# Optimization experiments

Hardware: AMD Instinct MI355X
Metric: run time of the kernel (lower is better)

The kernel has to match this reference:

```python
import jax, jax.numpy as jnp
import numpy as np

B, S, H, NH = 1, 2048, 2048, 32
HD = H // NH  # 64
DFF = 4 * H
EPS = 1e-5


def layer_norm(x, w, b):
    mu = jnp.mean(x, axis=-1, keepdims=True)
    var = jnp.var(x, axis=-1, keepdims=True)
    return (x - mu) * jax.lax.rsqrt(var + EPS) * w + b


def setup_inputs() -> dict:
    key = jax.random.key(0)
    ks = jax.random.split(key, 16)
    std = 0.02
    hidden_states = jax.random.normal(ks[0], (B, S, H), dtype=jnp.float32)
    # additive causal mask [1,1,S,S]
    causal = jnp.tril(jnp.ones((S, S), dtype=jnp.bool_))
    attention_mask = jnp.where(causal, 0.0, -1e9).astype(jnp.float32)[None, None]
    p = lambda k, shp: (jax.random.normal(k, shp, dtype=jnp.float32) * std)
    return {
        "hidden_states": hidden_states,
        "attention_mask": attention_mask,
        "ln1_w": jnp.ones((H,), jnp.float32), "ln1_b": jnp.zeros((H,), jnp.float32),
        "wq": p(ks[1], (H, H)), "bq": jnp.zeros((H,), jnp.float32),
        "wk": p(ks[2], (H, H)), "bk": jnp.zeros((H,), jnp.float32),
        "wv": p(ks[3], (H, H)), "bv": jnp.zeros((H,), jnp.float32),
        "wo": p(ks[4], (H, H)), "bo": jnp.zeros((H,), jnp.float32),
        "w1": p(ks[5], (H, DFF)), "b1": jnp.zeros((DFF,), jnp.float32),
        "w2": p(ks[6], (DFF, H)), "b2": jnp.zeros((H,), jnp.float32),
        "ln2_w": jnp.ones((H,), jnp.float32), "ln2_b": jnp.zeros((H,), jnp.float32),
    }


def reference(hidden_states, attention_mask, ln1_w, ln1_b, wq, bq, wk, bk, wv, bv,
              wo, bo, w1, b1, w2, b2, ln2_w, ln2_b):
    x = hidden_states
    # --- pre-norm attention ---
    residual = x
    h = layer_norm(x, ln1_w, ln1_b)
    scaling = HD ** -0.5
    q = (h @ wq + bq).reshape(B, S, NH, HD) * scaling
    k = (h @ wk + bk).reshape(B, S, NH, HD)
    v = (h @ wv + bv).reshape(B, S, NH, HD)
    scores = jnp.einsum('bqhd,bkhd->bhqk', q, k) + attention_mask
    p = jax.nn.softmax(scores, axis=-1)  # dropout is identity in eval
    attn = jnp.einsum('bhqk,bkhd->bqhd', p, v).reshape(B, S, H)
    attn = attn @ wo + bo
    x = residual + attn
    # --- pre-norm MLP ---
    residual = x
    h = layer_norm(x, ln2_w, ln2_b)
    h = jax.nn.gelu(h @ w1 + b1, approximate=False) @ w2 + b2
    return residual + h
```

## Files before the change

### kernel.cpp

```cpp
#include <hip/hip_runtime.h>
#include <math.h>

#define H 2048
#define S 2048
#define NH 32
#define HD 64
#define DFF 8192

typedef __attribute__((ext_vector_type(4))) float f32x4;
typedef __attribute__((ext_vector_type(8))) short short8;

static __device__ __forceinline__ ushort f2bf(float f) {
  unsigned u = __float_as_uint(f);
  u += 0x7fff + ((u >> 16) & 1);
  return (ushort)(u >> 16);
}

static __device__ __forceinline__ void gl_lds16(const ushort* g, ushort* l) {
  __builtin_amdgcn_global_load_lds(
      (__attribute__((address_space(1))) const void*)g,
      (__attribute__((address_space(3))) void*)l, 16, 0, 0);
}

__global__ __launch_bounds__(256) void transpose4_kernel(
    const float* __restrict__ w0, const float* __restrict__ w1,
    const float* __restrict__ w2, const float* __restrict__ w3,
    ushort* __restrict__ o0, ushort* __restrict__ o1,
    ushort* __restrict__ o2, ushort* __restrict__ o3) {
  __shared__ __align__(16) ushort tile[64][72];
  int z = blockIdx.z;
  const float* W = (z == 0) ? w0 : (z == 1) ? w1 : (z == 2) ? w2 : w3;
  ushort* Wt = (z == 0) ? o0 : (z == 1) ? o1 : (z == 2) ? o2 : o3;
  int n0 = blockIdx.x * 64, k0 = blockIdx.y * 64;
  int t = threadIdx.x;
  int lk = t >> 4;
  int ln4 = (t & 15) * 4;
#pragma unroll
  for (int p = 0; p < 4; p++) {
    int k = p * 16 + lk;
    float4 v = *reinterpret_cast<const float4*>(&W[(size_t)(k0 + k) * H + n0 + ln4]);
    float vv[4] = {v.x, v.y, v.z, v.w};
#pragma unroll
    for (int i = 0; i < 4; i++) {
      int row = ln4 + i;
      int slot = ((k >> 3) ^ (row & 7));
      tile[row][(slot << 3) + (k & 7)] = f2bf(vv[i]);
    }
  }
  __syncthreads();
  int n = t >> 2;
  int kq = (t & 3) * 8;
#pragma unroll
  for (int p = 0; p < 2; p++) {
    int kk = kq + p * 32;
    int slot = ((kk >> 3) ^ (n & 7));
    short8 o = *reinterpret_cast<const short8*>(&tile[n][slot << 3]);
    *reinterpret_cast<short8*>(&Wt[(size_t)(n0 + n) * H + k0 + kk]) = o;
  }
}

__global__ __launch_bounds__(256) void transpose_cast_kernel(
    const float* __restrict__ W, ushort* __restrict__ Wt, int K, int N) {
  __shared__ __align__(16) ushort tile[64][72];
  int n0 = blockIdx.x * 64, k0 = blockIdx.y * 64;
  int t = threadIdx.x;
  int lk = t >> 4;
  int ln4 = (t & 15) * 4;
#pragma unroll
  for (int p = 0; p < 4; p++) {
    int k = p * 16 + lk;
    float4 v = *reinterpret_cast<const float4*>(&W[(size_t)(k0 + k) * N + n0 + ln4]);
    float vv[4] = {v.x, v.y, v.z, v.w};
#pragma unroll
    for (int i = 0; i < 4; i++) {
      int row = ln4 + i;
      int slot = ((k >> 3) ^ (row & 7));
      tile[row][(slot << 3) + (k & 7)] = f2bf(vv[i]);
    }
  }
  __syncthreads();
  int n = t >> 2;
  int kq = (t & 3) * 8;
#pragma unroll
  for (int p = 0; p < 2; p++) {
    int kk = kq + p * 32;
    int slot = ((kk >> 3) ^ (n & 7));
    short8 o = *reinterpret_cast<const short8*>(&tile[n][slot << 3]);
    *reinterpret_cast<short8*>(&Wt[(size_t)(n0 + n) * K + k0 + kk]) = o;
  }
}

__global__ __launch_bounds__(256) void vtrans_kernel(
    const ushort* __restrict__ V, ushort* __restrict__ VT) {
  __shared__ ushort tile[32][33];
  int s0 = blockIdx.x * 32, d0 = blockIdx.y * 32;
  int tx = threadIdx.x & 31, ty = threadIdx.x >> 5;
#pragma unroll
  for (int i = 0; i < 4; i++)
    tile[ty * 4 + i][tx] = V[(size_t)(s0 + ty * 4 + i) * H + d0 + tx];
  __syncthreads();
#pragma unroll
  for (int i = 0; i < 4; i++)
    VT[(size_t)(d0 + ty * 4 + i) * S + s0 + tx] = tile[tx][ty * 4 + i];
}

__global__ __launch_bounds__(256) void biascat_kernel(
    const float* __restrict__ bq, const float* __restrict__ bk,
    const float* __restrict__ bv, float* __restrict__ o) {
  int t = blockIdx.x * 256 + threadIdx.x;
  o[t] = (t < H) ? bq[t] : (t < 2 * H) ? bk[t - H] : bv[t - 2 * H];
}

__global__ __launch_bounds__(256) void ln_kernel(
    const float* __restrict__ x, const float* __restrict__ w,
    const float* __restrict__ b, ushort* __restrict__ out) {
  int row = blockIdx.x, t = threadIdx.x;
  const float4* xr = reinterpret_cast<const float4*>(x + (size_t)row * H);
  float4 v0 = xr[t * 2], v1 = xr[t * 2 + 1];
  float s = v0.x + v0.y + v0.z + v0.w + v1.x + v1.y + v1.z + v1.w;
  float q = v0.x * v0.x + v0.y * v0.y + v0.z * v0.z + v0.w * v0.w +
            v1.x * v1.x + v1.y * v1.y + v1.z * v1.z + v1.w * v1.w;
#pragma unroll
  for (int off = 32; off > 0; off >>= 1) {
    s += __shfl_down(s, off, 64);
    q += __shfl_down(q, off, 64);
  }
  __shared__ float sm[8];
  int lane = t & 63, wv = t >> 6;
  if (lane == 0) { sm[wv] = s; sm[wv + 4] = q; }
  __syncthreads();
  s = sm[0] + sm[1] + sm[2] + sm[3];
  q = sm[4] + sm[5] + sm[6] + sm[7];
  float mu = s * (1.0f / H);
  float var = q * (1.0f / H) - mu * mu;
  float rs = rsqrtf(var + 1e-5f);
  const float4* wr = reinterpret_cast<const float4*>(w);
  const float4* br = reinterpret_cast<const float4*>(b);
  float4 w0 = wr[t * 2], w1v = wr[t * 2 + 1], b0 = br[t * 2], b1v = br[t * 2 + 1];
  short8 pk;
  pk[0] = (short)f2bf((v0.x - mu) * rs * w0.x + b0.x);
  pk[1] = (short)f2bf((v0.y - mu) * rs * w0.y + b0.y);
  pk[2] = (short)f2bf((v0.z - mu) * rs * w0.z + b0.z);
  pk[3] = (short)f2bf((v0.w - mu) * rs * w0.w + b0.w);
  pk[4] = (short)f2bf((v1.x - mu) * rs * w1v.x + b1v.x);
  pk[5] = (short)f2bf((v1.y - mu) * rs * w1v.y + b1v.y);
  pk[6] = (short)f2bf((v1.z - mu) * rs * w1v.z + b1v.z);
  pk[7] = (short)f2bf((v1.w - mu) * rs * w1v.w + b1v.w);
  *reinterpret_cast<short8*>(out + (size_t)row * H + t * 8) = pk;
}

__global__ __launch_bounds__(256) void combine4_kernel(
    const float* __restrict__ res, const float* __restrict__ p0,
    const float* __restrict__ p1, const float* __restrict__ p2,
    const float* __restrict__ p3, const float* __restrict__ bias,
    float* __restrict__ out) {
  size_t i = (size_t)blockIdx.x * 256 + threadIdx.x;
  float4 a = reinterpret_cast<const float4*>(res)[i];
  float4 c0 = reinterpret_cast<const float4*>(p0)[i];
  float4 c1 = reinterpret_cast<const float4*>(p1)[i];
  float4 c2 = reinterpret_cast<const float4*>(p2)[i];
  float4 c3 = reinterpret_cast<const float4*>(p3)[i];
  int col = (int)((i * 4) & (H - 1));
  float4 bb = *reinterpret_cast<const float4*>(bias + col);
  float4 o;
  o.x = a.x + c0.x + c1.x + c2.x + c3.x + bb.x;
  o.y = a.y + c0.y + c1.y + c2.y + c3.y + bb.y;
  o.z = a.z + c0.z + c1.z + c2.z + c3.z + bb.z;
  o.w = a.w + c0.w + c1.w + c2.w + c3.w + bb.w;
  reinterpret_cast<float4*>(out)[i] = o;
}

__global__ __launch_bounds__(256) void combine_ln_kernel(
    const float* __restrict__ res, const float* __restrict__ p0,
    const float* __restrict__ p1, const float* __restrict__ bias,
    const float* __restrict__ lw, const float* __restrict__ lb,
    float* __restrict__ xout, ushort* __restrict__ lnout) {
  int row = blockIdx.x, t = threadIdx.x;
  const float4* rr = reinterpret_cast<const float4*>(res + (size_t)row * H);
  const float4* r0 = reinterpret_cast<const float4*>(p0 + (size_t)row * H);
  const float4* r1 = reinterpret_cast<const float4*>(p1 + (size_t)row * H);
  const float4* bb = reinterpret_cast<const float4*>(bias);
  float4 a0 = rr[t * 2], a1 = rr[t * 2 + 1];
  float4 c0 = r0[t * 2], c1 = r0[t * 2 + 1];
  float4 d0 = r1[t * 2], d1 = r1[t * 2 + 1];
  float4 e0 = bb[t * 2], e1 = bb[t * 2 + 1];
  float4 v0, v1;
  v0.x = a0.x + c0.x + d0.x + e0.x;
  v0.y = a0.y + c0.y + d0.y + e0.y;
  v0.z = a0.z + c0.z + d0.z + e0.z;
  v0.w = a0.w + c0.w + d0.w + e0.w;
  v1.x = a1.x + c1.x + d1.x + e1.x;
  v1.y = a1.y + c1.y + d1.y + e1.y;
  v1.z = a1.z + c1.z + d1.z + e1.z;
  v1.w = a1.w + c1.w + d1.w + e1.w;
  float4* xo = reinterpret_cast<float4*>(xout + (size_t)row * H);
  xo[t * 2] = v0;
  xo[t * 2 + 1] = v1;
  float s = v0.x + v0.y + v0.z + v0.w + v1.x + v1.y + v1.z + v1.w;
  float q = v0.x * v0.x + v0.y * v0.y + v0.z * v0.z + v0.w * v0.w +
            v1.x * v1.x + v1.y * v1.y + v1.z * v1.z + v1.w * v1.w;
#pragma unroll
  for (int off = 32; off > 0; off >>= 1) {
    s += __shfl_down(s, off, 64);
    q += __shfl_down(q, off, 64);
  }
  __shared__ float sm[8];
  int lane = t & 63, wv = t >> 6;
  if (lane == 0) { sm[wv] = s; sm[wv + 4] = q; }
  __syncthreads();
  s = sm[0] + sm[1] + sm[2] + sm[3];
  q = sm[4] + sm[5] + sm[6] + sm[7];
  float mu = s * (1.0f / H);
  float var = q * (1.0f / H) - mu * mu;
  float rs = rsqrtf(var + 1e-5f);
  const float4* wr = reinterpret_cast<const float4*>(lw);
  const float4* br = reinterpret_cast<const float4*>(lb);
  float4 w0 = wr[t * 2], w1v = wr[t * 2 + 1], b0 = br[t * 2], b1v = br[t * 2 + 1];
  short8 pk;
  pk[0] = (short)f2bf((v0.x - mu) * rs * w0.x + b0.x);
  pk[1] = (short)f2bf((v0.y - mu) * rs * w0.y + b0.y);
  pk[2] = (short)f2bf((v0.z - mu) * rs * w0.z + b0.z);
  pk[3] = (short)f2bf((v0.w - mu) * rs * w0.w + b0.w);
  pk[4] = (short)f2bf((v1.x - mu) * rs * w1v.x + b1v.x);
  pk[5] = (short)f2bf((v1.y - mu) * rs * w1v.y + b1v.y);
  pk[6] = (short)f2bf((v1.z - mu) * rs * w1v.z + b1v.z);
  pk[7] = (short)f2bf((v1.w - mu) * rs * w1v.w + b1v.w);
  *reinterpret_cast<short8*>(lnout + (size_t)row * H + t * 8) = pk;
}

template <int MODE, int NI>
__global__ __launch_bounds__(512, 2) void gemm256_kernel(
    const ushort* __restrict__ A, const ushort* __restrict__ Bt,
    const float* __restrict__ bias,
    ushort* __restrict__ outb, float* __restrict__ outf,
    int M, int N, int lda, int kbeg, int klen) {
  constexpr int BN = NI * 64;
  constexpr int NH0 = (NI + 1) / 2;
  constexpr int NH1 = NI - NH0;
  constexpr int BQ0 = (NI + 1) / 2;
  __shared__ __align__(16) ushort As[2][256 * 64];
  __shared__ __align__(16) ushort Bs[2][BN * 64];
  int tid = threadIdx.x, lane = tid & 63, w = tid >> 6;
  int lm = lane & 15, kg = lane >> 4;
  int wr = w >> 2, wc = w & 3;
  int gx = gridDim.x, nwg = gx * gridDim.y;
  int orig = blockIdx.y * gx + blockIdx.x;
  int wg = (orig & 7) * (nwg >> 3) + (orig >> 3);
  int m0 = (wg % gx) * 256, n0 = (wg / gx) * BN;
  int kb0 = kbeg + blockIdx.z * klen;

  f32x4 acc[8][NI] = {};

  const ushort* srcA[4];
  const ushort* srcB[NI];
  int dbase[4];
#pragma unroll
  for (int q = 0; q < 4; q++) {
    int g = q * 512 + tid;
    int row = g >> 3, gc = g & 7;
    int col = (gc ^ (row & 7)) << 3;
    srcA[q] = A + (size_t)(m0 + row) * lda + kb0 + col;
    if (q < NI) srcB[q] = Bt + (size_t)(n0 + row) * lda + kb0 + col;
    dbase[q] = (q * 512 + w * 64) * 8;
  }

  const ushort* aB0 = &As[0][(wr * 128 + lm) * 64 + ((kg ^ (lm & 7)) << 3)];
  const ushort* aB1 = &As[0][(wr * 128 + lm) * 64 + (((4 + kg) ^ (lm & 7)) << 3)];
  const ushort* bB0 = &Bs[0][(wc * 16 * NI + lm) * 64 + ((kg ^ (lm & 7)) << 3)];
  const ushort* bB1 = &Bs[0][(wc * 16 * NI + lm) * 64 + (((4 + kg) ^ (lm & 7)) << 3)];

  int nK = klen >> 6;
#pragma unroll
  for (int q = 0; q < NI; q++) gl_lds16(srcB[q], &Bs[0][dbase[q]]);
  gl_lds16(srcA[0], &As[0][dbase[0]]);
  gl_lds16(srcA[2], &As[0][dbase[2]]);
  gl_lds16(srcA[1], &As[0][dbase[1]]);
  gl_lds16(srcA[3], &As[0][dbase[3]]);
  asm volatile("s_waitcnt vmcnt(2)" ::: "memory");
  __builtin_amdgcn_s_barrier();

  for (int kt = 0; kt < nK; kt++) {
    int cur = kt & 1, nxt = cur ^ 1;
    bool hn = (kt + 1 < nK);
    int ko = (kt + 1) << 6;
    const ushort* a0 = aB0 + cur * 16384;
    const ushort* a1 = aB1 + cur * 16384;
    const ushort* b0 = bB0 + cur * (BN * 64);
    const ushort* b1 = bB1 + cur * (BN * 64);

    short8 af[4][2], bf0[NH0][2], bf1[NH0][2];

#pragma unroll
    for (int i = 0; i < 4; i++) {
      af[i][0] = *reinterpret_cast<const short8*>(a0 + i * 1024);
      af[i][1] = *reinterpret_cast<const short8*>(a1 + i * 1024);
    }
#pragma unroll
    for (int n = 0; n < NH0; n++) {
      bf0[n][0] = *reinterpret_cast<const short8*>(b0 + n * 1024);
      bf0[n][1] = *reinterpret_cast<const short8*>(b1 + n * 1024);
    }
    if (hn) {
#pragma unroll
      for (int q = 0; q < BQ0; q++) gl_lds16(srcB[q] + ko, &Bs[nxt][dbase[q]]);
    }
    __builtin_amdgcn_s_barrier();
    asm volatile("s_waitcnt lgkmcnt(0)" ::: "memory");
    __builtin_amdgcn_sched_barrier(0);
    __builtin_amdgcn_s_setprio(1);
#pragma unroll
    for (int i = 0; i < 4; i++)
#pragma unroll
      for (int n = 0; n < NH0; n++)
#pragma unroll
        for (int s = 0; s < 2; s++)
          acc[i][n] = __builtin_amdgcn_mfma_f32_16x16x32_bf16(af[i][s], bf0[n][s], acc[i][n], 0, 0, 0);
    __builtin_amdgcn_s_setprio(0);
    __builtin_amdgcn_s_barrier();

#pragma unroll
    for (int n = 0; n < NH1; n++) {
      bf1[n][0] = *reinterpret_cast<const short8*>(b0 + (NH0 + n) * 1024);
      bf1[n][1] = *reinterpret_cast<const short8*>(b1 + (NH0 + n) * 1024);
    }
    if (hn) {
#pragma unroll
      for (int q = BQ0; q < NI; q++) gl_lds16(srcB[q] + ko, &Bs[nxt][dbase[q]]);
    }
    __builtin_amdgcn_s_barrier();
    asm volatile("s_waitcnt lgkmcnt(0)" ::: "memory");
    __builtin_amdgcn_sched_barrier(0);
    __builtin_amdgcn_s_setprio(1);
#pragma unroll
    for (int i = 0; i < 4; i++)
#pragma unroll
      for (int n = 0; n < NH1; n++)
#pragma unroll
        for (int s = 0; s < 2; s++)
          acc[i][NH0 + n] = __builtin_amdgcn_mfma_f32_16x16x32_bf16(af[i][s], bf1[n][s], acc[i][NH0 + n], 0, 0, 0);
    __builtin_amdgcn_s_setprio(0);
    if (hn) {
      if constexpr (NI == 4) asm volatile("s_waitcnt vmcnt(4)" ::: "memory");
      else if constexpr (NI == 3) asm volatile("s_waitcnt vmcnt(3)" ::: "memory");
      else asm volatile("s_waitcnt vmcnt(2)" ::: "memory");
    } else {
      asm volatile("s_waitcnt vmcnt(0)" ::: "memory");
    }
    __builtin_amdgcn_s_barrier();

#pragma unroll
    for (int i = 0; i < 4; i++) {
      af[i][0] = *reinterpret_cast<const short8*>(a0 + 4096 + i * 1024);
      af[i][1] = *reinterpret_cast<const short8*>(a1 + 4096 + i * 1024);
    }
    if (hn) {
      gl_lds16(srcA[0] + ko, &As[nxt][dbase[0]]);
      gl_lds16(srcA[2] + ko, &As[nxt][dbase[2]]);
    }
    __builtin_amdgcn_s_barrier();
    asm volatile("s_waitcnt lgkmcnt(0)" ::: "memory");
    __builtin_amdgcn_sched_barrier(0);
    __builtin_amdgcn_s_setprio(1);
#pragma unroll
    for (int i = 0; i < 4; i++)
#pragma unroll
      for (int n = 0; n < NH0; n++)
#pragma unroll
        for (int s = 0; s < 2; s++)
          acc[4 + i][n] = __builtin_amdgcn_mfma_f32_16x16x32_bf16(af[i][s], bf0[n][s], acc[4 + i][n], 0, 0, 0);
    __builtin_amdgcn_s_setprio(0);
    __builtin_amdgcn_s_barrier();

    if (hn) {
      gl_lds16(srcA[1] + ko, &As[nxt][dbase[1]]);
      gl_lds16(srcA[3] + ko, &As[nxt][dbase[3]]);
    }
    __builtin_amdgcn_s_barrier();
    __builtin_amdgcn_s_setprio(1);
#pragma unroll
    for (int i = 0; i < 4; i++)
#pragma unroll
      for (int n = 0; n < NH1; n++)
#pragma unroll
        for (int s = 0; s < 2; s++)
          acc[4 + i][NH0 + n] = __builtin_amdgcn_mfma_f32_16x16x32_bf16(af[i][s], bf1[n][s], acc[4 + i][NH0 + n], 0, 0, 0);
    __builtin_amdgcn_s_setprio(0);
    if (hn) asm volatile("s_waitcnt vmcnt(2)" ::: "memory");
    __builtin_amdgcn_s_barrier();
  }

#pragma unroll
  for (int mi = 0; mi < 8; mi++) {
#pragma unroll
    for (int ni = 0; ni < NI; ni++) {
#pragma unroll
      for (int r = 0; r < 4; r++) {
        int row = m0 + wr * 128 + mi * 16 + kg * 4 + r;
        int col = n0 + wc * 16 * NI + ni * 16 + lm;
        float v = acc[mi][ni][r];
        if (MODE == 0) {
          float t = v + bias[col];
          float sc = (col < H) ? 0.125f : 1.0f;
          size_t idx = (size_t)(col >> 11) * ((size_t)S * H) + (size_t)row * H + (col & (H - 1));
          outb[idx] = f2bf(t * sc);
        } else if (MODE == 1) {
          float t = v + bias[col];
          outb[(size_t)row * N + col] = f2bf(0.5f * t * (1.0f + erff(t * 0.70710678118f)));
        } else {
          int zs = blockIdx.z + ((blockIdx.z >> 1) << 1);
          outf[(size_t)zs * M * N + (size_t)row * N + col] = v;
        }
      }
    }
  }
}

__global__ __launch_bounds__(512) void attn_kernel(
    const ushort* __restrict__ Q, const ushort* __restrict__ Kmat,
    const ushort* __restrict__ VT, ushort* __restrict__ ctx) {
  __shared__ __align__(16) ushort Ks[2][128 * 64];
  __shared__ __align__(16) ushort Vs[2][64 * 128];
  __shared__ __align__(16) ushort Ps[8 * 16 * 64];
  int h = blockIdx.x;
  int x = blockIdx.y;
  int tid = threadIdx.x, lane = tid & 63, w = tid >> 6;
  int lm = lane & 15, kg = lane >> 4;

  int qbA = x, qbB = 15 - x;
  int tA = x + 1;
  const int nt = 17;

  short8 qa[2];
#pragma unroll
  for (int ks = 0; ks < 2; ks++)
    qa[ks] = *reinterpret_cast<const short8*>(
        Q + (size_t)(qbA * 128 + w * 16 + lm) * H + h * 64 + ks * 32 + kg * 8);

  float m_run[4], l_run[4];
  f32x4 o_acc[4] = {};
#pragma unroll
  for (int r = 0; r < 4; r++) { m_run[r] = -1e30f; l_run[r] = 0.f; }

  auto stage = [&](int kb, int buf) {
#pragma unroll
    for (int p = 0; p < 2; p++) {
      int gbase = p * 512 + w * 64;
      int gran = gbase + lane;
      int krow = gran >> 3, gk = gran & 7;
      gl_lds16(Kmat + (size_t)(kb * 128 + krow) * H + h * 64 + ((gk ^ (krow & 7)) << 3),
               &Ks[buf][gbase * 8]);
    }
#pragma unroll
    for (int p = 0; p < 2; p++) {
      int gbase = p * 512 + w * 64;
      int gran = gbase + lane;
      int vrow = gran >> 4, gv = gran & 15;
      gl_lds16(VT + (size_t)(h * 64 + vrow) * S + kb * 128 + ((gv ^ (vrow & 15)) << 3),
               &Vs[buf][gbase * 8]);
    }
  };

  stage(0, 0);
  __syncthreads();

  for (int t = 0; t < nt; t++) {
    int cur = t & 1;
    if (t + 1 < nt) {
      int tn = t + 1;
      stage((tn < tA) ? tn : tn - tA, cur ^ 1);
    }
    bool diag = (t == tA - 1) || (t == nt - 1);

    f32x4 sacc[8] = {};
#pragma unroll
    for (int j = 0; j < 8; j++) {
      int krow = j * 16 + lm;
#pragma unroll
      for (int ks = 0; ks < 2; ks++) {
        short8 kf = *reinterpret_cast<const short8*>(
            &Ks[cur][krow * 64 + (((ks * 4 + kg) ^ (lm & 7)) << 3)]);
        sacc[j] = __builtin_amdgcn_mfma_f32_16x16x32_bf16(qa[ks], kf, sacc[j], 0, 0, 0);
      }
    }
    if (diag) {
#pragma unroll
      for (int j = 0; j < 8; j++)
#pragma unroll
        for (int r = 0; r < 4; r++)
          if (j * 16 + lm > w * 16 + kg * 4 + r) sacc[j][r] = -1e30f;
    }

#pragma unroll
    for (int r = 0; r < 4; r++) {
      float mx = sacc[0][r];
#pragma unroll
      for (int j = 1; j < 8; j++) mx = fmaxf(mx, sacc[j][r]);
      mx = fmaxf(mx, __shfl_xor(mx, 1, 64));
      mx = fmaxf(mx, __shfl_xor(mx, 2, 64));
      mx = fmaxf(mx, __shfl_xor(mx, 4, 64));
      mx = fmaxf(mx, __shfl_xor(mx, 8, 64));
      float mnew = fmaxf(m_run[r], mx);
      float sc = __expf(m_run[r] - mnew);
      m_run[r] = mnew;
      float ps = 0.f;
#pragma unroll
      for (int j = 0; j < 8; j++) {
        float p = __expf(sacc[j][r] - mnew);
        sacc[j][r] = p;
        ps += p;
      }
      ps += __shfl_xor(ps, 1, 64);
      ps += __shfl_xor(ps, 2, 64);
      ps += __shfl_xor(ps, 4, 64);
      ps += __shfl_xor(ps, 8, 64);
      l_run[r] = l_run[r] * sc + ps;
#pragma unroll
      for (int jd = 0; jd < 4; jd++) o_acc[jd][r] *= sc;
    }

#pragma unroll
    for (int c = 0; c < 2; c++) {
#pragma unroll
      for (int jj = 0; jj < 4; jj++)
#pragma unroll
        for (int r = 0; r < 4; r++) {
          int rl = kg * 4 + r;
          int col = jj * 16 + lm;
          Ps[w * 1024 + rl * 64 + (((col >> 3) ^ (rl & 7)) << 3) + (col & 7)] =
              f2bf(sacc[c * 4 + jj][r]);
        }
      short8 pa[2];
#pragma unroll
      for (int ks = 0; ks < 2; ks++)
        pa[ks] = *reinterpret_cast<const short8*>(
            &Ps[w * 1024 + lm * 64 + (((ks * 4 + kg) ^ (lm & 7)) << 3)]);
#pragma unroll
      for (int jd = 0; jd < 4; jd++) {
        int d = jd * 16 + lm;
#pragma unroll
        for (int ks = 0; ks < 2; ks++) {
          short8 vf = *reinterpret_cast<const short8*>(
              &Vs[cur][d * 128 + (((c * 8 + ks * 4 + kg) ^ lm) << 3)]);
          o_acc[jd] = __builtin_amdgcn_mfma_f32_16x16x32_bf16(pa[ks], vf, o_acc[jd], 0, 0, 0);
        }
      }
    }

    if (t == tA - 1) {
#pragma unroll
      for (int jd = 0; jd < 4; jd++)
#pragma unroll
        for (int r = 0; r < 4; r++)
          ctx[(size_t)(qbA * 128 + w * 16 + kg * 4 + r) * H + h * 64 + jd * 16 + lm] =
              f2bf(o_acc[jd][r] / l_run[r]);
#pragma unroll
      for (int r = 0; r < 4; r++) { m_run[r] = -1e30f; l_run[r] = 0.f; }
#pragma unroll
      for (int jd = 0; jd < 4; jd++) o_acc[jd] = f32x4{0.f, 0.f, 0.f, 0.f};
#pragma unroll
      for (int ks = 0; ks < 2; ks++)
        qa[ks] = *reinterpret_cast<const short8*>(
            Q + (size_t)(qbB * 128 + w * 16 + lm) * H + h * 64 + ks * 32 + kg * 8);
    }
    __syncthreads();
  }

#pragma unroll
  for (int jd = 0; jd < 4; jd++)
#pragma unroll
    for (int r = 0; r < 4; r++)
      ctx[(size_t)(qbB * 128 + w * 16 + kg * 4 + r) * H + h * 64 + jd * 16 + lm] =
          f2bf(o_acc[jd][r] / l_run[r]);
}

extern "C" void kernel_launch(void* const* d_in, const int* in_sizes, int n_in,
                              void* d_out, int out_size, void* d_ws, size_t ws_size,
                              hipStream_t stream) {
  const float* x = (const float*)d_in[0];
  const float* ln1w = (const float*)d_in[2];
  const float* ln1b = (const float*)d_in[3];
  const float* wq = (const float*)d_in[4];
  const float* bq = (const float*)d_in[5];
  const float* wk = (const float*)d_in[6];
  const float* bk = (const float*)d_in[7];
  const float* wv = (const float*)d_in[8];
  const float* bv = (const float*)d_in[9];
  const float* wo = (const float*)d_in[10];
  const float* bo = (const float*)d_in[11];
  const float* w1 = (const float*)d_in[12];
  const float* b1 = (const float*)d_in[13];
  const float* w2 = (const float*)d_in[14];
  const float* b2 = (const float*)d_in[15];
  const float* ln2w = (const float*)d_in[16];
  const float* ln2b = (const float*)d_in[17];
  float* out = (float*)d_out;

  char* ws = (char*)d_ws;
  const size_t MB = 1024 * 1024;
  const size_t SH = (size_t)S * H;
  ushort* WT_QKV = (ushort*)(ws);
  ushort* WT_O = (ushort*)(ws + 24 * MB);
  ushort* WT_1 = (ushort*)(ws + 32 * MB);
  ushort* WT_2 = (ushort*)(ws + 64 * MB);
  ushort* LNO = (ushort*)(ws + 96 * MB);
  ushort* QKVB = (ushort*)(ws + 104 * MB);
  ushort* VTb = (ushort*)(ws + 128 * MB);
  ushort* CTX = (ushort*)(ws + 136 * MB);
  float* X1 = (float*)(ws + 144 * MB);
  float* BIASQ = (float*)(ws + 160 * MB);
  ushort* MID = (ushort*)(ws);
  float* SPA = (float*)(ws + 104 * MB);
  float* SPM = (float*)(ws + 32 * MB);

  transpose4_kernel<<<dim3(H / 64, H / 64, 4), 256, 0, stream>>>(
      wq, wk, wv, wo, WT_QKV, WT_QKV + SH, WT_QKV + 2 * SH, WT_O);
  transpose_cast_kernel<<<dim3(DFF / 64, H / 64), 256, 0, stream>>>(w1, WT_1, H, DFF);
  transpose_cast_kernel<<<dim3(H / 64, DFF / 64), 256, 0, stream>>>(w2, WT_2, DFF, H);
  biascat_kernel<<<3 * H / 256, 256, 0, stream>>>(bq, bk, bv, BIASQ);

  ln_kernel<<<S, 256, 0, stream>>>(x, ln1w, ln1b, LNO);

  gemm256_kernel<0, 3><<<dim3(S / 256, 3 * H / 192), 512, 0, stream>>>(
      LNO, WT_QKV, BIASQ, QKVB, nullptr, S, 3 * H, H, 0, H);

  vtrans_kernel<<<dim3(S / 32, H / 32), 256, 0, stream>>>(QKVB + 2 * SH, VTb);

  attn_kernel<<<dim3(NH, 8), 512, 0, stream>>>(QKVB, QKVB + SH, VTb, CTX);

  gemm256_kernel<3, 2><<<dim3(S / 256, H / 128, 2), 512, 0, stream>>>(
      CTX, WT_O, nullptr, nullptr, SPA, S, H, H, 0, H / 2);
  combine_ln_kernel<<<S, 256, 0, stream>>>(x, SPA, SPA + SH, bo, ln2w, ln2b, X1, LNO);

  gemm256_kernel<1, 4><<<dim3(S / 256, DFF / 256), 512, 0, stream>>>(
      LNO, WT_1, b1, MID, nullptr, S, DFF, H, 0, H);

  gemm256_kernel<3, 4><<<dim3(S / 256, H / 256, 4), 512, 0, stream>>>(
      MID, WT_2, nullptr, nullptr, SPM, S, H, DFF, 0, DFF / 4);
  combine4_kernel<<<SH / 1024, 256, 0, stream>>>(
      X1, SPM, SPM + SH, SPM + 4 * SH, SPM + 5 * SH, b2, out);
}
```

Measured before the change: 401.3 us.

## Merge weight transposes, fuse V transpose into QKV epilogue, retune FFN2 split-K

All weight transpose-casts now run in one launch, and the bias concat kernel is gone because the QKV GEMM epilogue reads bq/bk/bv directly. The V part of the QKV GEMM is written transposed straight into the VT buffer, which removes the separate vtrans kernel. FFN2 changes from a 4-way split-K with 256-wide tiles to a 2-way split with 128-wide tiles, so the final combine reads fewer partial buffers. The explicit lgkmcnt waits and sched barriers after the barriers in the GEMM main loop are removed, which relies on the compiler to insert the LDS waits correctly.

Result: no change. 396.4 us (-1.2%).

```diff
diff --git a/kernel.cpp b/kernel.cpp
--- a/kernel.cpp
+++ b/kernel.cpp
@@ -9,6 +9,7 @@
 
 typedef __attribute__((ext_vector_type(4))) float f32x4;
 typedef __attribute__((ext_vector_type(8))) short short8;
+typedef __attribute__((ext_vector_type(4))) short s16x4;
 
 static __device__ __forceinline__ ushort f2bf(float f) {
   unsigned u = __float_as_uint(f);
@@ -22,47 +23,32 @@
       (__attribute__((address_space(3))) void*)l, 16, 0, 0);
 }
 
-__global__ __launch_bounds__(256) void transpose4_kernel(
-    const float* __restrict__ w0, const float* __restrict__ w1,
-    const float* __restrict__ w2, const float* __restrict__ w3,
-    ushort* __restrict__ o0, ushort* __restrict__ o1,
-    ushort* __restrict__ o2, ushort* __restrict__ o3) {
+__global__ __launch_bounds__(256) void transpose_all_kernel(
+    const float* __restrict__ wq, const float* __restrict__ wk,
+    const float* __restrict__ wv, const float* __restrict__ wo,
+    const float* __restrict__ w1, const float* __restrict__ w2,
+    ushort* __restrict__ oQKV, ushort* __restrict__ oO,
+    ushort* __restrict__ o1, ushort* __restrict__ o2) {
   __shared__ __align__(16) ushort tile[64][72];
-  int z = blockIdx.z;
-  const float* W = (z == 0) ? w0 : (z == 1) ? w1 : (z == 2) ? w2 : w3;
-  ushort* Wt = (z == 0) ? o0 : (z == 1) ? o1 : (z == 2) ? o2 : o3;
-  int n0 = blockIdx.x * 64, k0 = blockIdx.y * 64;
-  int t = threadIdx.x;
-  int lk = t >> 4;
-  int ln4 = (t & 15) * 4;
-#pragma unroll
-  for (int p = 0; p < 4; p++) {
-    int k = p * 16 + lk;
-    float4 v = *reinterpret_cast<const float4*>(&W[(size_t)(k0 + k) * H + n0 + ln4]);
-    float vv[4] = {v.x, v.y, v.z, v.w};
-#pragma unroll
-    for (int i = 0; i < 4; i++) {
-      int row = ln4 + i;
-      int slot = ((k >> 3) ^ (row & 7));
-      tile[row][(slot << 3) + (k & 7)] = f2bf(vv[i]);
-    }
-  }
-  __syncthreads();
-  int n = t >> 2;
-  int kq = (t & 3) * 8;
-#pragma unroll
-  for (int p = 0; p < 2; p++) {
-    int kk = kq + p * 32;
-    int slot = ((kk >> 3) ^ (n & 7));
-    short8 o = *reinterpret_cast<const short8*>(&tile[n][slot << 3]);
-    *reinterpret_cast<short8*>(&Wt[(size_t)(n0 + n) * H + k0 + kk]) = o;
-  }
-}
-
-__global__ __launch_bounds__(256) void transpose_cast_kernel(
-    const float* __restrict__ W, ushort* __restrict__ Wt, int K, int N) {
-  __shared__ __align__(16) ushort tile[64][72];
-  int n0 = blockIdx.x * 64, k0 = blockIdx.y * 64;
+  int id = blockIdx.x;
+  const float* W;
+  ushort* Wt;
+  int K, N, bx, by;
+  if (id < 4096) {
+    int which = id >> 10, r = id & 1023;
+    bx = r & 31; by = r >> 5; K = H; N = H;
+    W = (which == 0) ? wq : (which == 1) ? wk : (which == 2) ? wv : wo;
+    Wt = (which == 3) ? oO : oQKV + (size_t)which * H * H;
+  } else if (id < 8192) {
+    int r = id - 4096;
+    bx = r & 127; by = r >> 7; K = H; N = DFF;
+    W = w1; Wt = o1;
+  } else {
+    int r = id - 8192;
+    bx = r & 31; by = r >> 5; K = DFF; N = H;
+    W = w2; Wt = o2;
+  }
+  int n0 = bx * 64, k0 = by * 64;
   int t = threadIdx.x;
   int lk = t >> 4;
   int ln4 = (t & 15) * 4;
@@ -88,27 +74,6 @@
     short8 o = *reinterpret_cast<const short8*>(&tile[n][slot << 3]);
     *reinterpret_cast<short8*>(&Wt[(size_t)(n0 + n) * K + k0 + kk]) = o;
   }
-}
-
-__global__ __launch_bounds__(256) void vtrans_kernel(
-    const ushort* __restrict__ V, ushort* __restrict__ VT) {
-  __shared__ ushort tile[32][33];
-  int s0 = blockIdx.x * 32, d0 = blockIdx.y * 32;
-  int tx = threadIdx.x & 31, ty = threadIdx.x >> 5;
-#pragma unroll
-  for (int i = 0; i < 4; i++)
-    tile[ty * 4 + i][tx] = V[(size_t)(s0 + ty * 4 + i) * H + d0 + tx];
-  __syncthreads();
-#pragma unroll
-  for (int i = 0; i < 4; i++)
-    VT[(size_t)(d0 + ty * 4 + i) * S + s0 + tx] = tile[tx][ty * 4 + i];
-}
-
-__global__ __launch_bounds__(256) void biascat_kernel(
-    const float* __restrict__ bq, const float* __restrict__ bk,
-    const float* __restrict__ bv, float* __restrict__ o) {
-  int t = blockIdx.x * 256 + threadIdx.x;
-  o[t] = (t < H) ? bq[t] : (t < 2 * H) ? bk[t - H] : bv[t - 2 * H];
 }
 
 __global__ __launch_bounds__(256) void ln_kernel(
@@ -149,24 +114,21 @@
   *reinterpret_cast<short8*>(out + (size_t)row * H + t * 8) = pk;
 }
 
-__global__ __launch_bounds__(256) void combine4_kernel(
+__global__ __launch_bounds__(256) void combine2_kernel(
     const float* __restrict__ res, const float* __restrict__ p0,
-    const float* __restrict__ p1, const float* __restrict__ p2,
-    const float* __restrict__ p3, const float* __restrict__ bias,
+    const float* __restrict__ p1, const float* __restrict__ bias,
     float* __restrict__ out) {
   size_t i = (size_t)blockIdx.x * 256 + threadIdx.x;
   float4 a = reinterpret_cast<const float4*>(res)[i];
   float4 c0 = reinterpret_cast<const float4*>(p0)[i];
   float4 c1 = reinterpret_cast<const float4*>(p1)[i];
-  float4 c2 = reinterpret_cast<const float4*>(p2)[i];
-  float4 c3 = reinterpret_cast<const float4*>(p3)[i];
   int col = (int)((i * 4) & (H - 1));
   float4 bb = *reinterpret_cast<const float4*>(bias + col);
   float4 o;
-  o.x = a.x + c0.x + c1.x + c2.x + c3.x + bb.x;
-  o.y = a.y + c0.y + c1.y + c2.y + c3.y + bb.y;
-  o.z = a.z + c0.z + c1.z + c2.z + c3.z + bb.z;
-  o.w = a.w + c0.w + c1.w + c2.w + c3.w + bb.w;
+  o.x = a.x + c0.x + c1.x + bb.x;
+  o.y = a.y + c0.y + c1.y + bb.y;
+  o.z = a.z + c0.z + c1.z + bb.z;
+  o.w = a.w + c0.w + c1.w + bb.w;
   reinterpret_cast<float4*>(out)[i] = o;
 }
 
@@ -231,8 +193,10 @@
 template <int MODE, int NI>
 __global__ __launch_bounds__(512, 2) void gemm256_kernel(
     const ushort* __restrict__ A, const ushort* __restrict__ Bt,
-    const float* __restrict__ bias,
-    ushort* __restrict__ outb, float* __restrict__ outf,
+    const float* __restrict__ bias, const float* __restrict__ biasB,
+    const float* __restrict__ biasC,
+    ushort* __restrict__ outb, ushort* __restrict__ outbV,
+    float* __restrict__ outf,
     int M, int N, int lda, int kbeg, int klen) {
   constexpr int BN = NI * 64;
   constexpr int NH0 = (NI + 1) / 2;
@@ -305,8 +269,6 @@
       for (int q = 0; q < BQ0; q++) gl_lds16(srcB[q] + ko, &Bs[nxt][dbase[q]]);
     }
     __builtin_amdgcn_s_barrier();
-    asm volatile("s_waitcnt lgkmcnt(0)" ::: "memory");
-    __builtin_amdgcn_sched_barrier(0);
     __builtin_amdgcn_s_setprio(1);
 #pragma unroll
     for (int i = 0; i < 4; i++)
@@ -328,8 +290,6 @@
       for (int q = BQ0; q < NI; q++) gl_lds16(srcB[q] + ko, &Bs[nxt][dbase[q]]);
     }
     __builtin_amdgcn_s_barrier();
-    asm volatile("s_waitcnt lgkmcnt(0)" ::: "memory");
-    __builtin_amdgcn_sched_barrier(0);
     __builtin_amdgcn_s_setprio(1);
 #pragma unroll
     for (int i = 0; i < 4; i++)
@@ -358,8 +318,6 @@
       gl_lds16(srcA[2] + ko, &As[nxt][dbase[2]]);
     }
     __builtin_amdgcn_s_barrier();
-    asm volatile("s_waitcnt lgkmcnt(0)" ::: "memory");
-    __builtin_amdgcn_sched_barrier(0);
     __builtin_amdgcn_s_setprio(1);
 #pragma unroll
     for (int i = 0; i < 4; i++)
@@ -393,23 +351,34 @@
   for (int mi = 0; mi < 8; mi++) {
 #pragma unroll
     for (int ni = 0; ni < NI; ni++) {
-#pragma unroll
-      for (int r = 0; r < 4; r++) {
-        int row = m0 + wr * 128 + mi * 16 + kg * 4 + r;
-        int col = n0 + wc * 16 * NI + ni * 16 + lm;
-        float v = acc[mi][ni][r];
-        if (MODE == 0) {
-          float t = v + bias[col];
+      int row0 = m0 + wr * 128 + mi * 16 + kg * 4;
+      int col = n0 + wc * 16 * NI + ni * 16 + lm;
+      f32x4 v4 = acc[mi][ni];
+      if (MODE == 0) {
+        if (col < 2 * H) {
+          float bb = (col < H) ? bias[col] : biasB[col - H];
           float sc = (col < H) ? 0.125f : 1.0f;
-          size_t idx = (size_t)(col >> 11) * ((size_t)S * H) + (size_t)row * H + (col & (H - 1));
-          outb[idx] = f2bf(t * sc);
-        } else if (MODE == 1) {
-          float t = v + bias[col];
-          outb[(size_t)row * N + col] = f2bf(0.5f * t * (1.0f + erff(t * 0.70710678118f)));
+          size_t base = (size_t)(col >> 11) * ((size_t)S * H) + (col & (H - 1));
+#pragma unroll
+          for (int r = 0; r < 4; r++)
+            outb[base + (size_t)(row0 + r) * H] = f2bf((v4[r] + bb) * sc);
         } else {
-          int zs = blockIdx.z + ((blockIdx.z >> 1) << 1);
-          outf[(size_t)zs * M * N + (size_t)row * N + col] = v;
+          float bb = biasC[col - 2 * H];
+          s16x4 pk;
+#pragma unroll
+          for (int r = 0; r < 4; r++) pk[r] = (short)f2bf(v4[r] + bb);
+          *reinterpret_cast<s16x4*>(outbV + (size_t)(col - 2 * H) * S + row0) = pk;
         }
+      } else if (MODE == 1) {
+#pragma unroll
+        for (int r = 0; r < 4; r++) {
+          float t = v4[r] + bias[col];
+          outb[(size_t)(row0 + r) * N + col] = f2bf(0.5f * t * (1.0f + erff(t * 0.70710678118f)));
+        }
+      } else {
+#pragma unroll
+        for (int r = 0; r < 4; r++)
+          outf[(size_t)blockIdx.z * M * N + (size_t)(row0 + r) * N + col] = v4[r];
       }
     }
   }
@@ -607,35 +576,28 @@
   ushort* VTb = (ushort*)(ws + 128 * MB);
   ushort* CTX = (ushort*)(ws + 136 * MB);
   float* X1 = (float*)(ws + 144 * MB);
-  float* BIASQ = (float*)(ws + 160 * MB);
   ushort* MID = (ushort*)(ws);
   float* SPA = (float*)(ws + 104 * MB);
   float* SPM = (float*)(ws + 32 * MB);
 
-  transpose4_kernel<<<dim3(H / 64, H / 64, 4), 256, 0, stream>>>(
-      wq, wk, wv, wo, WT_QKV, WT_QKV + SH, WT_QKV + 2 * SH, WT_O);
-  transpose_cast_kernel<<<dim3(DFF / 64, H / 64), 256, 0, stream>>>(w1, WT_1, H, DFF);
-  transpose_cast_kernel<<<dim3(H / 64, DFF / 64), 256, 0, stream>>>(w2, WT_2, DFF, H);
-  biascat_kernel<<<3 * H / 256, 256, 0, stream>>>(bq, bk, bv, BIASQ);
+  transpose_all_kernel<<<12288, 256, 0, stream>>>(
+      wq, wk, wv, wo, w1, w2, WT_QKV, WT_O, WT_1, WT_2);
 
   ln_kernel<<<S, 256, 0, stream>>>(x, ln1w, ln1b, LNO);
 
   gemm256_kernel<0, 3><<<dim3(S / 256, 3 * H / 192), 512, 0, stream>>>(
-      LNO, WT_QKV, BIASQ, QKVB, nullptr, S, 3 * H, H, 0, H);
-
-  vtrans_kernel<<<dim3(S / 32, H / 32), 256, 0, stream>>>(QKVB + 2 * SH, VTb);
+      LNO, WT_QKV, bq, bk, bv, QKVB, VTb, nullptr, S, 3 * H, H, 0, H);
 
   attn_kernel<<<dim3(NH, 8), 512, 0, stream>>>(QKVB, QKVB + SH, VTb, CTX);
 
   gemm256_kernel<3, 2><<<dim3(S / 256, H / 128, 2), 512, 0, stream>>>(
-      CTX, WT_O, nullptr, nullptr, SPA, S, H, H, 0, H / 2);
+      CTX, WT_O, nullptr, nullptr, nullptr, nullptr, nullptr, SPA, S, H, H, 0, H / 2);
   combine_ln_kernel<<<S, 256, 0, stream>>>(x, SPA, SPA + SH, bo, ln2w, ln2b, X1, LNO);
 
   gemm256_kernel<1, 4><<<dim3(S / 256, DFF / 256), 512, 0, stream>>>(
-      LNO, WT_1, b1, MID, nullptr, S, DFF, H, 0, H);
-
-  gemm256_kernel<3, 4><<<dim3(S / 256, H / 256, 4), 512, 0, stream>>>(
-      MID, WT_2, nullptr, nullptr, SPM, S, H, DFF, 0, DFF / 4);
-  combine4_kernel<<<SH / 1024, 256, 0, stream>>>(
-      X1, SPM, SPM + SH, SPM + 4 * SH, SPM + 5 * SH, b2, out);
-}
+      LNO, WT_1, b1, nullptr, nullptr, MID, nullptr, nullptr, S, DFF, H, 0, H);
+
+  gemm256_kernel<3, 2><<<dim3(S / 256, H / 128, 2), 512, 0, stream>>>(
+      MID, WT_2, nullptr, nullptr, nullptr, nullptr, nullptr, SPM, S, H, DFF, 0, DFF / 2);
+  combine2_kernel<<<SH / 1024, 256, 0, stream>>>(X1, SPM, SPM + SH, b2, out);
+}
```
